# Performance work log

Measured on AMD Instinct MI355X. Metric: run time of the kernel, lower is better.

Reference implementation:

```python
import jax, jax.numpy as jnp
import numpy as np

S, B, I, H = 512, 64, 512, 1024

def _linear_params(key, out_dim, in_dim):
    kw, kb = jax.random.split(key)
    bound = 1.0 / np.sqrt(in_dim)
    W = jax.random.uniform(kw, (out_dim, in_dim), jnp.float32, -bound, bound)
    b = jax.random.uniform(kb, (out_dim,), jnp.float32, -bound, bound)
    return W, b

def setup_inputs() -> dict:
    key = jax.random.key(0)
    ks = jax.random.split(key, 9)
    x = jax.random.normal(ks[0], (S, B, I), jnp.float32)
    h = jnp.zeros((1, B, H), jnp.float32)
    c = jnp.zeros((1, B, H), jnp.float32)
    Wfx, bfx = _linear_params(ks[1], H, I)
    Wfh, bfh = _linear_params(ks[2], H, H)
    Wix, bix = _linear_params(ks[3], H, I)
    Wih, bih = _linear_params(ks[4], H, H)
    Wox, b_ox = _linear_params(ks[5], H, I)
    Woh, boh = _linear_params(ks[6], H, H)
    Wcx, bcx = _linear_params(ks[7], H, I)
    Wch, bch = _linear_params(ks[8], H, H)
    return dict(x=x, h=h, c=c, Wfx=Wfx, bfx=bfx, Wfh=Wfh, bfh=bfh,
                Wix=Wix, bix=bix, Wih=Wih, bih=bih,
                Wox=Wox, b_ox=b_ox, Woh=Woh, boh=boh,
                Wcx=Wcx, bcx=bcx, Wch=Wch, bch=bch)

def reference(x, h, c, Wfx, bfx, Wfh, bfh, Wix, bix, Wih, bih,
              Wox, b_ox, Woh, boh, Wcx, bcx, Wch, bch):
    # Initial states: sum over layer dim as in the original forward.
    h0 = h.sum(0)  # [B, H]
    c0 = c.sum(0)  # [B, H]
    # Precompute all input-to-gate projections in one batched GEMM each. [S,B,H]
    fx = jnp.einsum('sbi,hi->sbh', x, Wfx) + bfx
    ix = jnp.einsum('sbi,hi->sbh', x, Wix) + bix
    ox = jnp.einsum('sbi,hi->sbh', x, Wox) + b_ox
    cx = jnp.einsum('sbi,hi->sbh', x, Wcx) + bcx

    def step(carry, gates):
        hp, cp = carry
        fxt, ixt, oxt, cxt = gates
        f = jax.nn.sigmoid(fxt + hp @ Wfh.T + bfh)
        i = jax.nn.sigmoid(ixt + hp @ Wih.T + bih)
        o = jax.nn.sigmoid(oxt + hp @ Woh.T + boh)
        cn = f * cp + i * jnp.tanh(cxt + hp @ Wch.T + bch)
        hn = o * jnp.tanh(cn)
        return (hn, cn), hn

    (h_last, c_last), h_seq = jax.lax.scan(step, (h0, c0), (fx, ix, ox, cx))
    return h_seq, h_last, c_last
```

## Files before the change

### kernel.cpp

```cpp
#include <hip/hip_runtime.h>
#include <math.h>

#define SS 512
#define BB 64
#define II 512
#define HH 1024

typedef __attribute__((ext_vector_type(8))) __bf16 bf16x8;
typedef __attribute__((ext_vector_type(4))) float f32x4;

#define WPACK_ELEMS (256u * 48u * 64u * 8u)
#define HBF_ELEMS   (BB * HH)

struct StepParams {
  const float* x;
  const __bf16* wpack;
  const __bf16* hbf_in;
  __bf16* hbf_out;
  float* cbuf;
  const float* bx[4];
  const float* bh[4];
  float* out;
};

__global__ __launch_bounds__(1024) void lstm_step_mfma(StepParams p, int s) {
  __shared__ float part[4][4][16][17];
  __shared__ float pre[4][16][17];

  const int wb = blockIdx.x;
  const int t = threadIdx.x;
  const int w = t >> 6;
  const int lane = t & 63;
  const int bg = w & 3;
  const int ks = w >> 2;

  const int kof  = (lane >> 4) * 8;
  const int bcol = bg * 16 + (lane & 15);

  const __bf16* ap  = p.wpack + (((size_t)wb * 48) * 64 + lane) * 8;
  const __bf16* bhp = p.hbf_in + (size_t)bcol * HH + kof;
  const float*  bxp = p.x + ((size_t)s * BB + bcol) * II + kof;

  f32x4 acc = {0.f, 0.f, 0.f, 0.f};

#pragma unroll
  for (int j = 0; j < 8; ++j) {
    const int it = ks + 4 * j;
    bf16x8 a = *(const bf16x8*)(ap + (size_t)it * 512);
    bf16x8 b = *(const bf16x8*)(bhp + it * 32);
    acc = __builtin_amdgcn_mfma_f32_16x16x32_bf16(a, b, acc, 0, 0, 0);
  }
#pragma unroll
  for (int j = 0; j < 4; ++j) {
    const int it = 32 + ks + 4 * j;
    bf16x8 a = *(const bf16x8*)(ap + (size_t)it * 512);
    const float* xp = bxp + (it - 32) * 32;
    float4 x0 = *(const float4*)(xp);
    float4 x1 = *(const float4*)(xp + 4);
    bf16x8 b;
    b[0] = (__bf16)x0.x; b[1] = (__bf16)x0.y; b[2] = (__bf16)x0.z; b[3] = (__bf16)x0.w;
    b[4] = (__bf16)x1.x; b[5] = (__bf16)x1.y; b[6] = (__bf16)x1.z; b[7] = (__bf16)x1.w;
    acc = __builtin_amdgcn_mfma_f32_16x16x32_bf16(a, b, acc, 0, 0, 0);
  }

  const int drow = (lane >> 4) * 4;
  part[ks][bg][drow + 0][lane & 15] = acc[0];
  part[ks][bg][drow + 1][lane & 15] = acc[1];
  part[ks][bg][drow + 2][lane & 15] = acc[2];
  part[ks][bg][drow + 3][lane & 15] = acc[3];
  __syncthreads();

  {
    const int rbg = t >> 8;
    const int row = (t >> 4) & 15;
    const int bc  = t & 15;
    pre[rbg][row][bc] = part[0][rbg][row][bc] + part[1][rbg][row][bc]
                      + part[2][rbg][row][bc] + part[3][rbg][row][bc];
  }
  __syncthreads();

  if (t < 256) {
    const int b    = t >> 2;
    const int hsub = t & 3;
    const int hg   = wb * 4 + hsub;
    const int bg2  = b >> 4;
    const int bc   = b & 15;

    float pf = pre[bg2][ 0 + hsub][bc] + p.bx[0][hg] + p.bh[0][hg];
    float pi = pre[bg2][ 4 + hsub][bc] + p.bx[1][hg] + p.bh[1][hg];
    float po = pre[bg2][ 8 + hsub][bc] + p.bx[2][hg] + p.bh[2][hg];
    float pc = pre[bg2][12 + hsub][bc] + p.bx[3][hg] + p.bh[3][hg];

    float fg = 1.f / (1.f + __expf(-pf));
    float ig = 1.f / (1.f + __expf(-pi));
    float og = 1.f / (1.f + __expf(-po));
    float cg = tanhf(pc);

    const size_t ci = (size_t)b * HH + hg;
    float cp = p.cbuf[ci];
    float cn = fg * cp + ig * cg;
    float hn = og * tanhf(cn);

    p.out[(size_t)s * BB * HH + ci] = hn;
    p.hbf_out[ci] = (__bf16)hn;
    p.cbuf[ci] = cn;
    if (s == SS - 1) {
      p.out[(size_t)SS * BB * HH + ci] = hn;
      p.out[(size_t)SS * BB * HH + BB * HH + ci] = cn;
    }
  }
}

struct PackParams {
  const float* Wh[4];
  const float* Wx[4];
  __bf16* wpack;
};

__global__ __launch_bounds__(256) void pack_weights(PackParams p) {
  const int wb = blockIdx.x;
  const int t = threadIdx.x;
  const int it2 = t >> 6;
  const int lane = t & 63;
  const int r16 = lane & 15;
  const int g = r16 >> 2;
  const int hrow = wb * 4 + (r16 & 3);
  const int kof = (lane >> 4) * 8;
  for (int itb = 0; itb < 12; ++itb) {
    const int it = itb * 4 + it2;
    const float* src;
    if (it < 32) src = p.Wh[g] + (size_t)hrow * HH + it * 32 + kof;
    else         src = p.Wx[g] + (size_t)hrow * II + (it - 32) * 32 + kof;
    float4 s0 = *(const float4*)(src);
    float4 s1 = *(const float4*)(src + 4);
    bf16x8 v;
    v[0] = (__bf16)s0.x; v[1] = (__bf16)s0.y; v[2] = (__bf16)s0.z; v[3] = (__bf16)s0.w;
    v[4] = (__bf16)s1.x; v[5] = (__bf16)s1.y; v[6] = (__bf16)s1.z; v[7] = (__bf16)s1.w;
    *(bf16x8*)(p.wpack + (((size_t)wb * 48 + it) * 64 + lane) * 8) = v;
  }
}

__global__ __launch_bounds__(256) void prep_state(const float* h0, const float* c0,
                                                  __bf16* hbf0, float* cbuf) {
  const int i = blockIdx.x * 256 + threadIdx.x;
  hbf0[i] = (__bf16)h0[i];
  cbuf[i] = c0[i];
}

extern "C" void kernel_launch(void* const* d_in, const int* in_sizes, int n_in,
                              void* d_out, int out_size, void* d_ws, size_t ws_size,
                              hipStream_t stream) {
  (void)in_sizes; (void)n_in; (void)out_size; (void)ws_size;

  __bf16* wsb = (__bf16*)d_ws;
  __bf16* wpack = wsb;
  __bf16* hbf0 = wsb + WPACK_ELEMS;
  __bf16* hbf1 = hbf0 + HBF_ELEMS;
  float*  cbuf = (float*)(wsb + WPACK_ELEMS + 2 * HBF_ELEMS);

  PackParams pk;
  pk.Wx[0] = (const float*)d_in[3];  pk.Wh[0] = (const float*)d_in[5];
  pk.Wx[1] = (const float*)d_in[7];  pk.Wh[1] = (const float*)d_in[9];
  pk.Wx[2] = (const float*)d_in[11]; pk.Wh[2] = (const float*)d_in[13];
  pk.Wx[3] = (const float*)d_in[15]; pk.Wh[3] = (const float*)d_in[17];
  pk.wpack = wpack;

  StepParams p;
  p.x = (const float*)d_in[0];
  p.wpack = wpack;
  p.cbuf = cbuf;
  p.bx[0] = (const float*)d_in[4];  p.bh[0] = (const float*)d_in[6];
  p.bx[1] = (const float*)d_in[8];  p.bh[1] = (const float*)d_in[10];
  p.bx[2] = (const float*)d_in[12]; p.bh[2] = (const float*)d_in[14];
  p.bx[3] = (const float*)d_in[16]; p.bh[3] = (const float*)d_in[18];
  p.out = (float*)d_out;

  pack_weights<<<dim3(256), dim3(256), 0, stream>>>(pk);
  prep_state<<<dim3(256), dim3(256), 0, stream>>>(
      (const float*)d_in[1], (const float*)d_in[2], hbf0, cbuf);

  for (int s = 0; s < SS; ++s) {
    p.hbf_in  = (s & 1) ? hbf1 : hbf0;
    p.hbf_out = (s & 1) ? hbf0 : hbf1;
    lstm_step_mfma<<<dim3(256), dim3(1024), 0, stream>>>(p, s);
  }
}
```

Measured before the change: 6.493 ms.

## Fuse all timesteps into one persistent cooperative kernel with grid sync

Replaces 512 per-step kernel launches with a single cooperative kernel that loops over time and uses grid-wide sync between steps. Weight fragments are loaded into registers once, and the cell state and summed biases stay in registers across steps, so per-step weight and state reloads are removed. This depends on all 256 blocks of 1024 threads being co-resident, and grid.sync has its own latency; it also raises register pressure.

```diff
diff --git a/kernel.cpp b/kernel.cpp
--- a/kernel.cpp
+++ b/kernel.cpp
@@ -1,5 +1,8 @@
 #include <hip/hip_runtime.h>
+#include <hip/hip_cooperative_groups.h>
 #include <math.h>
+
+namespace cg = cooperative_groups;
 
 #define SS 512
 #define BB 64
@@ -12,18 +15,20 @@
 #define WPACK_ELEMS (256u * 48u * 64u * 8u)
 #define HBF_ELEMS   (BB * HH)
 
-struct StepParams {
+struct PersistParams {
   const float* x;
   const __bf16* wpack;
-  const __bf16* hbf_in;
-  __bf16* hbf_out;
-  float* cbuf;
+  __bf16* hbf0;
+  __bf16* hbf1;
+  const float* c0;
   const float* bx[4];
   const float* bh[4];
   float* out;
 };
 
-__global__ __launch_bounds__(1024) void lstm_step_mfma(StepParams p, int s) {
+__global__ __launch_bounds__(1024, 4) void lstm_persist(PersistParams p) {
+  cg::grid_group grid = cg::this_grid();
+
   __shared__ float part[4][4][16][17];
   __shared__ float pre[4][16][17];
 
@@ -37,77 +42,94 @@
   const int kof  = (lane >> 4) * 8;
   const int bcol = bg * 16 + (lane & 15);
 
-  const __bf16* ap  = p.wpack + (((size_t)wb * 48) * 64 + lane) * 8;
-  const __bf16* bhp = p.hbf_in + (size_t)bcol * HH + kof;
-  const float*  bxp = p.x + ((size_t)s * BB + bcol) * II + kof;
-
-  f32x4 acc = {0.f, 0.f, 0.f, 0.f};
-
-#pragma unroll
-  for (int j = 0; j < 8; ++j) {
-    const int it = ks + 4 * j;
-    bf16x8 a = *(const bf16x8*)(ap + (size_t)it * 512);
-    bf16x8 b = *(const bf16x8*)(bhp + it * 32);
-    acc = __builtin_amdgcn_mfma_f32_16x16x32_bf16(a, b, acc, 0, 0, 0);
+  const __bf16* ap = p.wpack + (((size_t)wb * 48) * 64 + lane) * 8;
+  bf16x8 afr[12];
+#pragma unroll
+  for (int j = 0; j < 8; ++j)
+    afr[j] = *(const bf16x8*)(ap + (size_t)(ks + 4 * j) * 512);
+#pragma unroll
+  for (int j = 0; j < 4; ++j)
+    afr[8 + j] = *(const bf16x8*)(ap + (size_t)(32 + ks + 4 * j) * 512);
+
+  const int eb    = t >> 2;
+  const int hsub  = t & 3;
+  const int hg    = wb * 4 + hsub;
+  const int ebg   = eb >> 4;
+  const int ebc   = eb & 15;
+  float creg = 0.f, bsum0 = 0.f, bsum1 = 0.f, bsum2 = 0.f, bsum3 = 0.f;
+  if (t < 256) {
+    const size_t ci = (size_t)eb * HH + hg;
+    creg  = p.c0[ci];
+    bsum0 = p.bx[0][hg] + p.bh[0][hg];
+    bsum1 = p.bx[1][hg] + p.bh[1][hg];
+    bsum2 = p.bx[2][hg] + p.bh[2][hg];
+    bsum3 = p.bx[3][hg] + p.bh[3][hg];
   }
-#pragma unroll
-  for (int j = 0; j < 4; ++j) {
-    const int it = 32 + ks + 4 * j;
-    bf16x8 a = *(const bf16x8*)(ap + (size_t)it * 512);
-    const float* xp = bxp + (it - 32) * 32;
-    float4 x0 = *(const float4*)(xp);
-    float4 x1 = *(const float4*)(xp + 4);
-    bf16x8 b;
-    b[0] = (__bf16)x0.x; b[1] = (__bf16)x0.y; b[2] = (__bf16)x0.z; b[3] = (__bf16)x0.w;
-    b[4] = (__bf16)x1.x; b[5] = (__bf16)x1.y; b[6] = (__bf16)x1.z; b[7] = (__bf16)x1.w;
-    acc = __builtin_amdgcn_mfma_f32_16x16x32_bf16(a, b, acc, 0, 0, 0);
-  }
 
   const int drow = (lane >> 4) * 4;
-  part[ks][bg][drow + 0][lane & 15] = acc[0];
-  part[ks][bg][drow + 1][lane & 15] = acc[1];
-  part[ks][bg][drow + 2][lane & 15] = acc[2];
-  part[ks][bg][drow + 3][lane & 15] = acc[3];
-  __syncthreads();
-
-  {
-    const int rbg = t >> 8;
-    const int row = (t >> 4) & 15;
-    const int bc  = t & 15;
-    pre[rbg][row][bc] = part[0][rbg][row][bc] + part[1][rbg][row][bc]
-                      + part[2][rbg][row][bc] + part[3][rbg][row][bc];
-  }
-  __syncthreads();
-
-  if (t < 256) {
-    const int b    = t >> 2;
-    const int hsub = t & 3;
-    const int hg   = wb * 4 + hsub;
-    const int bg2  = b >> 4;
-    const int bc   = b & 15;
-
-    float pf = pre[bg2][ 0 + hsub][bc] + p.bx[0][hg] + p.bh[0][hg];
-    float pi = pre[bg2][ 4 + hsub][bc] + p.bx[1][hg] + p.bh[1][hg];
-    float po = pre[bg2][ 8 + hsub][bc] + p.bx[2][hg] + p.bh[2][hg];
-    float pc = pre[bg2][12 + hsub][bc] + p.bx[3][hg] + p.bh[3][hg];
-
-    float fg = 1.f / (1.f + __expf(-pf));
-    float ig = 1.f / (1.f + __expf(-pi));
-    float og = 1.f / (1.f + __expf(-po));
-    float cg = tanhf(pc);
-
-    const size_t ci = (size_t)b * HH + hg;
-    float cp = p.cbuf[ci];
-    float cn = fg * cp + ig * cg;
-    float hn = og * tanhf(cn);
-
-    p.out[(size_t)s * BB * HH + ci] = hn;
-    p.hbf_out[ci] = (__bf16)hn;
-    p.cbuf[ci] = cn;
-    if (s == SS - 1) {
-      p.out[(size_t)SS * BB * HH + ci] = hn;
-      p.out[(size_t)SS * BB * HH + BB * HH + ci] = cn;
-    }
+
+#pragma unroll 1
+  for (int s = 0; s < SS; ++s) {
+    const __bf16* hbin = ((s & 1) ? p.hbf1 : p.hbf0) + (size_t)bcol * HH + kof;
+    const float*  bxp  = p.x + ((size_t)s * BB + bcol) * II + kof;
+
+    f32x4 acc = {0.f, 0.f, 0.f, 0.f};
+#pragma unroll
+    for (int j = 0; j < 8; ++j) {
+      bf16x8 b = *(const bf16x8*)(hbin + (ks + 4 * j) * 32);
+      acc = __builtin_amdgcn_mfma_f32_16x16x32_bf16(afr[j], b, acc, 0, 0, 0);
+    }
+#pragma unroll
+    for (int j = 0; j < 4; ++j) {
+      const float* xp = bxp + (ks + 4 * j) * 32;
+      float4 x0 = *(const float4*)(xp);
+      float4 x1 = *(const float4*)(xp + 4);
+      bf16x8 b;
+      b[0] = (__bf16)x0.x; b[1] = (__bf16)x0.y; b[2] = (__bf16)x0.z; b[3] = (__bf16)x0.w;
+      b[4] = (__bf16)x1.x; b[5] = (__bf16)x1.y; b[6] = (__bf16)x1.z; b[7] = (__bf16)x1.w;
+      acc = __builtin_amdgcn_mfma_f32_16x16x32_bf16(afr[8 + j], b, acc, 0, 0, 0);
+    }
+
+    part[ks][bg][drow + 0][lane & 15] = acc[0];
+    part[ks][bg][drow + 1][lane & 15] = acc[1];
+    part[ks][bg][drow + 2][lane & 15] = acc[2];
+    part[ks][bg][drow + 3][lane & 15] = acc[3];
+    __syncthreads();
+
+    {
+      const int rbg = t >> 8;
+      const int row = (t >> 4) & 15;
+      const int bc  = t & 15;
+      pre[rbg][row][bc] = part[0][rbg][row][bc] + part[1][rbg][row][bc]
+                        + part[2][rbg][row][bc] + part[3][rbg][row][bc];
+    }
+    __syncthreads();
+
+    if (t < 256) {
+      float pf = pre[ebg][ 0 + hsub][ebc] + bsum0;
+      float pi = pre[ebg][ 4 + hsub][ebc] + bsum1;
+      float po = pre[ebg][ 8 + hsub][ebc] + bsum2;
+      float pc = pre[ebg][12 + hsub][ebc] + bsum3;
+
+      float fg = 1.f / (1.f + __expf(-pf));
+      float ig = 1.f / (1.f + __expf(-pi));
+      float og = 1.f / (1.f + __expf(-po));
+      float cg_ = tanhf(pc);
+
+      float cn = fg * creg + ig * cg_;
+      float hn = og * tanhf(cn);
+      creg = cn;
+
+      const size_t ci = (size_t)eb * HH + hg;
+      p.out[(size_t)s * BB * HH + ci] = hn;
+      ((s & 1) ? p.hbf0 : p.hbf1)[ci] = (__bf16)hn;
+      if (s == SS - 1) {
+        p.out[(size_t)SS * BB * HH + ci] = hn;
+        p.out[(size_t)SS * BB * HH + BB * HH + ci] = cn;
+      }
+    }
+
+    grid.sync();
   }
 }
 
@@ -140,11 +162,9 @@
   }
 }
 
-__global__ __launch_bounds__(256) void prep_state(const float* h0, const float* c0,
-                                                  __bf16* hbf0, float* cbuf) {
+__global__ __launch_bounds__(256) void prep_state(const float* h0, __bf16* hbf0) {
   const int i = blockIdx.x * 256 + threadIdx.x;
   hbf0[i] = (__bf16)h0[i];
-  cbuf[i] = c0[i];
 }
 
 extern "C" void kernel_launch(void* const* d_in, const int* in_sizes, int n_in,
@@ -156,7 +176,6 @@
   __bf16* wpack = wsb;
   __bf16* hbf0 = wsb + WPACK_ELEMS;
   __bf16* hbf1 = hbf0 + HBF_ELEMS;
-  float*  cbuf = (float*)(wsb + WPACK_ELEMS + 2 * HBF_ELEMS);
 
   PackParams pk;
   pk.Wx[0] = (const float*)d_in[3];  pk.Wh[0] = (const float*)d_in[5];
@@ -165,10 +184,12 @@
   pk.Wx[3] = (const float*)d_in[15]; pk.Wh[3] = (const float*)d_in[17];
   pk.wpack = wpack;
 
-  StepParams p;
+  PersistParams p;
   p.x = (const float*)d_in[0];
   p.wpack = wpack;
-  p.cbuf = cbuf;
+  p.hbf0 = hbf0;
+  p.hbf1 = hbf1;
+  p.c0 = (const float*)d_in[2];
   p.bx[0] = (const float*)d_in[4];  p.bh[0] = (const float*)d_in[6];
   p.bx[1] = (const float*)d_in[8];  p.bh[1] = (const float*)d_in[10];
   p.bx[2] = (const float*)d_in[12]; p.bh[2] = (const float*)d_in[14];
@@ -176,12 +197,9 @@
   p.out = (float*)d_out;
 
   pack_weights<<<dim3(256), dim3(256), 0, stream>>>(pk);
-  prep_state<<<dim3(256), dim3(256), 0, stream>>>(
-      (const float*)d_in[1], (const float*)d_in[2], hbf0, cbuf);
-
-  for (int s = 0; s < SS; ++s) {
-    p.hbf_in  = (s & 1) ? hbf1 : hbf0;
-    p.hbf_out = (s & 1) ? hbf0 : hbf1;
-    lstm_step_mfma<<<dim3(256), dim3(1024), 0, stream>>>(p, s);
-  }
-}
+  prep_state<<<dim3(256), dim3(256), 0, stream>>>((const float*)d_in[1], hbf0);
+
+  void* kargs[] = {&p};
+  hipLaunchCooperativeKernel((const void*)lstm_persist, dim3(256), dim3(1024),
+                             kargs, 0, stream);
+}
```

Measured after the change: 20.10 ms. +209.6%, slower.
